# Kernel optimization log

Measured on AMD Instinct MI355X. Metric: run time of the kernel, lower is better.

## Reference

```python
import jax, jax.numpy as jnp
import numpy as np

N_NODES = 100_000
N_EDGES = 3_200_000
F_IN, F_HID, F_OUT = 128, 128, 128
MLP_HID, MLP_OUT = 256, 64


def setup_inputs() -> dict:
    key = jax.random.key(0)
    ks = jax.random.split(key, 11)
    def w(k, shape):
        fan_in = shape[0]
        return jax.random.normal(k, shape, jnp.float32) / jnp.sqrt(jnp.float32(fan_in))
    return {
        'x':   jax.random.normal(ks[0], (N_NODES, F_IN), jnp.float32),
        'src': jax.random.randint(ks[1], (N_EDGES,), 0, N_NODES, jnp.int32),
        'dst': jax.random.randint(ks[2], (N_EDGES,), 0, N_NODES, jnp.int32),
        'w1':  w(ks[3], (F_IN, F_HID)),  'b1': jnp.zeros((F_HID,), jnp.float32),
        'w2':  w(ks[4], (F_HID, F_OUT)), 'b2': jnp.zeros((F_OUT,), jnp.float32),
        'wm1': w(ks[5], (F_OUT, MLP_HID)), 'bm1': jnp.zeros((MLP_HID,), jnp.float32),
        'wm2': w(ks[6], (MLP_HID, MLP_OUT)), 'bm2': jnp.zeros((MLP_OUT,), jnp.float32),
    }


def reference(x, src, dst, w1, b1, w2, b2, wm1, bm1, wm2, bm2):
    n = x.shape[0]
    ones = jnp.ones(src.shape[0], x.dtype)
    # DGL GraphConv norm='both': clamp degrees to >=1, symmetric D^-1/2 A D^-1/2
    out_norm = jnp.clip(jax.ops.segment_sum(ones, src, num_segments=n), 1.0) ** -0.5
    in_norm = jnp.clip(jax.ops.segment_sum(ones, dst, num_segments=n), 1.0) ** -0.5

    def gconv(h, w, b):
        msg = (h * out_norm[:, None])[src]                       # [E, F] gather
        agg = jax.ops.segment_sum(msg, dst, num_segments=n)      # [N, F] scatter-add
        return (agg * in_norm[:, None]) @ w + b

    h = jax.nn.relu(gconv(x, w1, b1))   # conv1 + relu (dropout is identity in eval)
    h = jax.nn.relu(gconv(h, w2, b2))   # conv2 + relu
    h = jax.nn.relu(h @ wm1 + bm1)      # MLP hidden layer
    return h @ wm2 + bm2                # MLP output (no final activation)
```

## Files before the change

kernel.cpp:

```cpp
#include <hip/hip_runtime.h>
#include <hip/hip_bf16.h>
#include <cstdint>

__device__ __forceinline__ unsigned short f2b(float f) {
    union { float f; unsigned int i; } v; v.f = f;
    unsigned int i = v.i;
    unsigned int r = (i + 0x7FFFu + ((i >> 16) & 1u)) >> 16;
    return (unsigned short)r;
}
__device__ __forceinline__ float b2f_lo(unsigned int p) {
    union { unsigned int i; float f; } v; v.i = p << 16; return v.f;
}
__device__ __forceinline__ float b2f_hi(unsigned int p) {
    union { unsigned int i; float f; } v; v.i = p & 0xFFFF0000u; return v.f;
}
__device__ __forceinline__ unsigned int pack2(float a, float b) {
    return (unsigned int)f2b(a) | ((unsigned int)f2b(b) << 16);
}

typedef __attribute__((__ext_vector_type__(8))) __bf16 bf16x8;
typedef __attribute__((__ext_vector_type__(4))) float  f32x4;

#define N_NODES 100000
#define N_EDGES 3200000
#define NBUCK   400
#define BSZ     250

__global__ void k_hist2(const int* __restrict__ src, const int* __restrict__ dst,
                        int* __restrict__ gcntA, int* __restrict__ gcntB, int E) {
    __shared__ int hA[NBUCK], hB[NBUCK];
    int t = threadIdx.x;
    for (int j = t; j < NBUCK; j += 256) { hA[j] = 0; hB[j] = 0; }
    __syncthreads();
    for (int i = blockIdx.x * blockDim.x + t; i < E; i += gridDim.x * blockDim.x) {
        atomicAdd(&hA[dst[i] / BSZ], 1);
        atomicAdd(&hB[src[i] / BSZ], 1);
    }
    __syncthreads();
    for (int j = t; j < NBUCK; j += 256) {
        if (hA[j]) atomicAdd(&gcntA[j], hA[j]);
        if (hB[j]) atomicAdd(&gcntB[j], hB[j]);
    }
}

__global__ void k_scan_coarse(const int* __restrict__ gcntA, const int* __restrict__ gcntB,
                              int* __restrict__ gbaseA, int* __restrict__ gbaseB,
                              int* __restrict__ gcurA, int* __restrict__ gcurB,
                              int* __restrict__ offsets) {
    __shared__ int pA[512], pB[512];
    int t = threadIdx.x;
    int vA = (t < NBUCK) ? gcntA[t] : 0;
    int vB = (t < NBUCK) ? gcntB[t] : 0;
    pA[t] = vA; pB[t] = vB;
    __syncthreads();
    for (int d = 1; d < 512; d <<= 1) {
        int a = (t >= d) ? pA[t - d] : 0;
        int b = (t >= d) ? pB[t - d] : 0;
        __syncthreads();
        pA[t] += a; pB[t] += b;
        __syncthreads();
    }
    if (t < NBUCK) {
        gbaseA[t] = pA[t] - vA; gcurA[t] = pA[t] - vA;
        gbaseB[t] = pB[t] - vB; gcurB[t] = pB[t] - vB;
    }
    if (t == 511) {
        gbaseA[NBUCK] = pA[511];
        gbaseB[NBUCK] = pB[511];
        offsets[N_NODES] = pA[511];
    }
}

__global__ void k_scatter(const int* __restrict__ src, const int* __restrict__ dst,
                          int* __restrict__ gcurA, int* __restrict__ gcurB,
                          unsigned* __restrict__ pairs, unsigned short* __restrict__ keysB,
                          int E) {
    __shared__ int hA[NBUCK], hB[NBUCK], baA[NBUCK], baB[NBUCK], lcA[NBUCK], lcB[NBUCK];
    int t = threadIdx.x;
    const int CHUNK = 12500;
    int lo = blockIdx.x * CHUNK, hi = min(lo + CHUNK, E);
    for (int j = t; j < NBUCK; j += 256) { hA[j] = 0; hB[j] = 0; }
    __syncthreads();
    for (int i = lo + t; i < hi; i += 256) {
        atomicAdd(&hA[dst[i] / BSZ], 1);
        atomicAdd(&hB[src[i] / BSZ], 1);
    }
    __syncthreads();
    for (int j = t; j < NBUCK; j += 256) {
        baA[j] = hA[j] ? atomicAdd(&gcurA[j], hA[j]) : 0;
        lcA[j] = 0;
        baB[j] = hB[j] ? atomicAdd(&gcurB[j], hB[j]) : 0;
        lcB[j] = 0;
    }
    __syncthreads();
    for (int i = lo + t; i < hi; i += 256) {
        int s = src[i], d = dst[i];
        int bA = d / BSZ;
        int l  = atomicAdd(&lcA[bA], 1);
        pairs[baA[bA] + l] = ((unsigned)(d - bA * BSZ) << 17) | (unsigned)s;
        int bB = s / BSZ;
        int l2 = atomicAdd(&lcB[bB], 1);
        keysB[baB[bB] + l2] = (unsigned short)(s - bB * BSZ);
    }
}

__global__ void k_csr_bucket(const unsigned* __restrict__ pairs, const int* __restrict__ gbaseA,
                             int* __restrict__ offsets, float* __restrict__ in_norm,
                             int* __restrict__ esrc) {
    __shared__ int hist[256], scan[256], curs[256];
    int b = blockIdx.x, t = threadIdx.x;
    int node0 = b * BSZ;
    int bstart = gbaseA[b], bend = gbaseA[b + 1];
    if (t < 256) hist[t] = 0;
    __syncthreads();
    for (int i = bstart + t; i < bend; i += 512)
        atomicAdd(&hist[pairs[i] >> 17], 1);
    __syncthreads();
    if (t < 256) scan[t] = hist[t];
    __syncthreads();
    for (int d = 1; d < 256; d <<= 1) {
        int v = (t < 256 && t >= d) ? scan[t - d] : 0;
        __syncthreads();
        if (t < 256) scan[t] += v;
        __syncthreads();
    }
    if (t < BSZ) {
        int excl = scan[t] - hist[t];
        offsets[node0 + t] = bstart + excl;
        in_norm[node0 + t] = rsqrtf((float)max(hist[t], 1));
        curs[t] = excl;
    }
    __syncthreads();
    for (int i = bstart + t; i < bend; i += 512) {
        unsigned p = pairs[i];
        int d = (int)(p >> 17);
        int l = atomicAdd(&curs[d], 1);
        esrc[bstart + l] = (int)(p & 0x1FFFFu);
    }
}

__global__ void k_sortwave(const int* __restrict__ offsets, int* __restrict__ esrc, int N) {
    int node = blockIdx.x * 4 + (threadIdx.x >> 6);
    if (node >= N) return;
    int lane = threadIdx.x & 63;
    int lo = offsets[node], hi = offsets[node + 1];
    int len = hi - lo;
    if (len <= 1) return;
    const int INF = 0x7FFFFFFF;
    if (len <= 64) {
        int v0 = (lane < len) ? esrc[lo + lane] : INF;
#pragma unroll
        for (int k = 2; k <= 64; k <<= 1) {
#pragma unroll
            for (int d = 32; d > 0; d >>= 1) {
                if (d >= k) continue;
                int w0 = __shfl_xor(v0, d, 64);
                bool up = ((lane & k) == 0);
                bool lower = ((lane & d) == 0);
                v0 = (lower == up) ? min(v0, w0) : max(v0, w0);
            }
        }
        if (lane < len) esrc[lo + lane] = v0;
        return;
    }
    int v0 = (lane < len) ? esrc[lo + lane] : INF;
    int v1 = (64 + lane < len) ? esrc[lo + 64 + lane] : INF;
#pragma unroll
    for (int k = 2; k <= 128; k <<= 1) {
#pragma unroll
        for (int d = 64; d > 0; d >>= 1) {
            if (d >= k) continue;
            if (d == 64) {
                int a = min(v0, v1), b = max(v0, v1);
                v0 = a; v1 = b;
            } else {
                int w0 = __shfl_xor(v0, d, 64);
                int w1 = __shfl_xor(v1, d, 64);
                bool up0 = ((lane & k) == 0);
                bool up1 = (((64 + lane) & k) == 0);
                bool lower = ((lane & d) == 0);
                v0 = (lower == up0) ? min(v0, w0) : max(v0, w0);
                v1 = (lower == up1) ? min(v1, w1) : max(v1, w1);
            }
        }
    }
    if (lane < len) esrc[lo + lane] = v0;
    if (64 + lane < len) esrc[lo + 64 + lane] = v1;
}

__global__ void k_count_scale(const unsigned short* __restrict__ keys,
                              const int* __restrict__ gbaseB,
                              const float4* __restrict__ x4, float* __restrict__ out_norm,
                              uint2* __restrict__ xs) {
    __shared__ int hist[256];
    __shared__ float onl[BSZ];
    int b = blockIdx.x, t = threadIdx.x;
    int node0 = b * BSZ;
    int bstart = gbaseB[b], bend = gbaseB[b + 1];
    if (t < 256) hist[t] = 0;
    __syncthreads();
    for (int i = bstart + t; i < bend; i += 512)
        atomicAdd(&hist[keys[i]], 1);
    __syncthreads();
    if (t < BSZ) {
        float on = rsqrtf((float)max(hist[t], 1));
        onl[t] = on;
        out_norm[node0 + t] = on;
    }
    __syncthreads();
    size_t base4 = (size_t)node0 * 32;
    for (int i = t; i < BSZ * 32; i += 512) {
        float on = onl[i >> 5];
        float4 v = x4[base4 + i];
        uint2 o;
        o.x = pack2(v.x * on, v.y * on);
        o.y = pack2(v.z * on, v.w * on);
        xs[base4 + i] = o;
    }
}

__global__ void k_transpose4(const float* __restrict__ w1, const float* __restrict__ w2,
                             const float* __restrict__ wm1, const float* __restrict__ wm2,
                             unsigned short* __restrict__ t1, unsigned short* __restrict__ t2,
                             unsigned short* __restrict__ tm1, unsigned short* __restrict__ tm2) {
    int i = blockIdx.x * blockDim.x + threadIdx.x;
    const float* w; unsigned short* t; int N, idx;
    if (i < 16384)       { w = w1;  t = t1;  N = 128; idx = i; }
    else if (i < 32768)  { w = w2;  t = t2;  N = 128; idx = i - 16384; }
    else if (i < 65536)  { w = wm1; t = tm1; N = 256; idx = i - 32768; }
    else if (i < 81920)  { w = wm2; t = tm2; N = 64;  idx = i - 65536; }
    else return;
    int K = (i < 65536) ? 128 : 256;
    int k = idx / N, n = idx - k * N;
    t[(size_t)n * K + k] = f2b(w[idx]);
}

#define AGG_ADD(p)                                                              \
        a0 += b2f_lo(p.x); a1 += b2f_hi(p.x);                                   \
        a2 += b2f_lo(p.y); a3 += b2f_hi(p.y);                                   \
        a4 += b2f_lo(p.z); a5 += b2f_hi(p.z);                                   \
        a6 += b2f_lo(p.w); a7 += b2f_hi(p.w);

#define AGG_NODE_BODY(node)                                                     \
    int lo = offsets[node], hi = offsets[node + 1];                             \
    float a0 = 0.f, a1 = 0.f, a2 = 0.f, a3 = 0.f,                               \
          a4 = 0.f, a5 = 0.f, a6 = 0.f, a7 = 0.f;                               \
    int k = lo + g;                                                             \
    for (; k + 12 < hi; k += 16) {                                              \
        int s0 = esrc[k];                                                       \
        int s1 = esrc[k + 4];                                                   \
        int s2 = esrc[k + 8];                                                   \
        int s3 = esrc[k + 12];                                                  \
        uint4 p0 = feat[(size_t)s0 * 16 + c];                                   \
        uint4 p1 = feat[(size_t)s1 * 16 + c];                                   \
        uint4 p2 = feat[(size_t)s2 * 16 + c];                                   \
        uint4 p3 = feat[(size_t)s3 * 16 + c];                                   \
        AGG_ADD(p0) AGG_ADD(p1) AGG_ADD(p2) AGG_ADD(p3)                         \
    }                                                                           \
    for (; k < hi; k += 4) {                                                    \
        int s = esrc[k];                                                        \
        uint4 p = feat[(size_t)s * 16 + c];                                     \
        AGG_ADD(p)                                                              \
    }                                                                           \
    a0 += __shfl_xor(a0, 16, 64); a0 += __shfl_xor(a0, 32, 64);                 \
    a1 += __shfl_xor(a1, 16, 64); a1 += __shfl_xor(a1, 32, 64);                 \
    a2 += __shfl_xor(a2, 16, 64); a2 += __shfl_xor(a2, 32, 64);                 \
    a3 += __shfl_xor(a3, 16, 64); a3 += __shfl_xor(a3, 32, 64);                 \
    a4 += __shfl_xor(a4, 16, 64); a4 += __shfl_xor(a4, 32, 64);                 \
    a5 += __shfl_xor(a5, 16, 64); a5 += __shfl_xor(a5, 32, 64);                 \
    a6 += __shfl_xor(a6, 16, 64); a6 += __shfl_xor(a6, 32, 64);                 \
    a7 += __shfl_xor(a7, 16, 64); a7 += __shfl_xor(a7, 32, 64);

__global__ __launch_bounds__(256, 8)
void k_conv(const int* __restrict__ offsets, const int* __restrict__ esrc,
            const uint4* __restrict__ feat, const float* __restrict__ in_norm,
            const unsigned short* __restrict__ WT, const float* __restrict__ bias,
            const float* __restrict__ row_scale, unsigned short* __restrict__ C,
            int N) {
    __shared__ __align__(16) unsigned short A[32][136];
    int wv = threadIdx.x >> 6, lane = threadIdx.x & 63;
    int row0 = blockIdx.x * 32;
    int g = lane >> 4, c = lane & 15;

    for (int i = 0; i < 8; ++i) {
        int nl = wv * 8 + i;
        int node = row0 + nl;
        AGG_NODE_BODY(node)
        if (g == 0) {
            float inn = in_norm[node];
            uint4 o;
            o.x = pack2(a0 * inn, a1 * inn);
            o.y = pack2(a2 * inn, a3 * inn);
            o.z = pack2(a4 * inn, a5 * inn);
            o.w = pack2(a6 * inn, a7 * inn);
            *(uint4*)&A[nl][c * 8] = o;
        }
    }
    __syncthreads();

    int m = lane & 15, q = lane >> 4;
    const unsigned short* b0 = WT + (size_t)(wv * 32 + m) * 128 + q * 8;
    const unsigned short* b1 = b0 + (size_t)16 * 128;
    f32x4 acc00 = {0.f, 0.f, 0.f, 0.f}, acc10 = {0.f, 0.f, 0.f, 0.f};
    f32x4 acc01 = {0.f, 0.f, 0.f, 0.f}, acc11 = {0.f, 0.f, 0.f, 0.f};
#pragma unroll
    for (int k = 0; k < 128; k += 32) {
        bf16x8 bf0 = *(const bf16x8*)(b0 + k);
        bf16x8 bf1 = *(const bf16x8*)(b1 + k);
        bf16x8 af0 = *(const bf16x8*)&A[m][q * 8 + k];
        bf16x8 af1 = *(const bf16x8*)&A[16 + m][q * 8 + k];
        acc00 = __builtin_amdgcn_mfma_f32_16x16x32_bf16(af0, bf0, acc00, 0, 0, 0);
        acc10 = __builtin_amdgcn_mfma_f32_16x16x32_bf16(af1, bf0, acc10, 0, 0, 0);
        acc01 = __builtin_amdgcn_mfma_f32_16x16x32_bf16(af0, bf1, acc01, 0, 0, 0);
        acc11 = __builtin_amdgcn_mfma_f32_16x16x32_bf16(af1, bf1, acc11, 0, 0, 0);
    }
    __syncthreads();

    int col0 = wv * 32 + m;
    int col1 = col0 + 16;
    float bc0 = bias[col0], bc1 = bias[col1];
#pragma unroll
    for (int r = 0; r < 4; r++) {
        int rl = q * 4 + r;
        int rr = row0 + rl, rr1 = rr + 16;
        float v00 = fmaxf(acc00[r] + bc0, 0.f);
        float v10 = fmaxf(acc10[r] + bc0, 0.f);
        float v01 = fmaxf(acc01[r] + bc1, 0.f);
        float v11 = fmaxf(acc11[r] + bc1, 0.f);
        float s0 = row_scale[rr], s1 = row_scale[rr1];
        v00 *= s0; v01 *= s0; v10 *= s1; v11 *= s1;
        A[rl][col0]      = f2b(v00);
        A[rl][col1]      = f2b(v01);
        A[rl + 16][col0] = f2b(v10);
        A[rl + 16][col1] = f2b(v11);
    }
    __syncthreads();
#pragma unroll
    for (int it = 0; it < 2; ++it) {
        int idx = it * 256 + (int)threadIdx.x;
        int row = idx >> 4, seg = idx & 15;
        uint4 v = *(const uint4*)&A[row][seg * 8];
        *(uint4*)&C[(size_t)(row0 + row) * 128 + seg * 8] = v;
    }
}

__global__ __launch_bounds__(256, 8)
void k_conv2_mlp(const int* __restrict__ offsets, const int* __restrict__ esrc,
                 const uint4* __restrict__ feat, const float* __restrict__ in_norm,
                 const unsigned short* __restrict__ WT2, const float* __restrict__ b2,
                 const unsigned short* __restrict__ WTM1, const float* __restrict__ bm1,
                 const unsigned short* __restrict__ WTM2, const float* __restrict__ bm2,
                 float* __restrict__ out, int N) {
    __shared__ __align__(16) unsigned short smem[8704];
    unsigned short (*H1)[136] = (unsigned short(*)[136])(smem);
    unsigned short (*A)[136]  = (unsigned short(*)[136])(smem + 4352);
    unsigned short (*H2)[136] = (unsigned short(*)[136])(smem + 4352);

    int wv = threadIdx.x >> 6, lane = threadIdx.x & 63;
    int row0 = blockIdx.x * 32;
    int g = lane >> 4, c = lane & 15;

    for (int i = 0; i < 8; ++i) {
        int nl = wv * 8 + i;
        int node = row0 + nl;
        AGG_NODE_BODY(node)
        if (g == 0) {
            float inn = in_norm[node];
            uint4 o;
            o.x = pack2(a0 * inn, a1 * inn);
            o.y = pack2(a2 * inn, a3 * inn);
            o.z = pack2(a4 * inn, a5 * inn);
            o.w = pack2(a6 * inn, a7 * inn);
            *(uint4*)&A[nl][c * 8] = o;
        }
    }
    __syncthreads();

    int m = lane & 15, q = lane >> 4;

    {
        const unsigned short* bb0 = WT2 + (size_t)(wv * 32 + m) * 128 + q * 8;
        const unsigned short* bb1 = bb0 + (size_t)16 * 128;
        f32x4 acc00 = {0.f, 0.f, 0.f, 0.f}, acc10 = {0.f, 0.f, 0.f, 0.f};
        f32x4 acc01 = {0.f, 0.f, 0.f, 0.f}, acc11 = {0.f, 0.f, 0.f, 0.f};
#pragma unroll
        for (int k = 0; k < 128; k += 32) {
            bf16x8 bf0 = *(const bf16x8*)(bb0 + k);
            bf16x8 bf1 = *(const bf16x8*)(bb1 + k);
            bf16x8 af0 = *(const bf16x8*)&A[m][q * 8 + k];
            bf16x8 af1 = *(const bf16x8*)&A[16 + m][q * 8 + k];
            acc00 = __builtin_amdgcn_mfma_f32_16x16x32_bf16(af0, bf0, acc00, 0, 0, 0);
            acc10 = __builtin_amdgcn_mfma_f32_16x16x32_bf16(af1, bf0, acc10, 0, 0, 0);
            acc01 = __builtin_amdgcn_mfma_f32_16x16x32_bf16(af0, bf1, acc01, 0, 0, 0);
            acc11 = __builtin_amdgcn_mfma_f32_16x16x32_bf16(af1, bf1, acc11, 0, 0, 0);
        }
        int col0 = wv * 32 + m;
        int col1 = col0 + 16;
        float bc0 = b2[col0], bc1 = b2[col1];
#pragma unroll
        for (int r = 0; r < 4; r++) {
            int rl = q * 4 + r;
            H1[rl][col0]      = f2b(fmaxf(acc00[r] + bc0, 0.f));
            H1[rl][col1]      = f2b(fmaxf(acc01[r] + bc1, 0.f));
            H1[rl + 16][col0] = f2b(fmaxf(acc10[r] + bc0, 0.f));
            H1[rl + 16][col1] = f2b(fmaxf(acc11[r] + bc1, 0.f));
        }
    }
    __syncthreads();

    f32x4 macc0 = {0.f, 0.f, 0.f, 0.f}, macc1 = {0.f, 0.f, 0.f, 0.f};
    int colo = wv * 16 + m;
    const unsigned short* bp2 = WTM2 + (size_t)colo * 256 + q * 8;
#pragma unroll
    for (int half = 0; half < 2; ++half) {
#pragma unroll
        for (int cb = 0; cb < 2; cb++) {
            int colh = half * 128 + wv * 32 + cb * 16 + m;
            const unsigned short* bp = WTM1 + (size_t)colh * 128 + q * 8;
            f32x4 acc0 = {0.f, 0.f, 0.f, 0.f};
            f32x4 acc1 = {0.f, 0.f, 0.f, 0.f};
#pragma unroll
            for (int s = 0; s < 4; s++) {
                bf16x8 bfr = *(const bf16x8*)(bp + s * 32);
                bf16x8 ha0 = *(const bf16x8*)&H1[m][s * 32 + q * 8];
                bf16x8 ha1 = *(const bf16x8*)&H1[m + 16][s * 32 + q * 8];
                acc0 = __builtin_amdgcn_mfma_f32_16x16x32_bf16(ha0, bfr, acc0, 0, 0, 0);
                acc1 = __builtin_amdgcn_mfma_f32_16x16x32_bf16(ha1, bfr, acc1, 0, 0, 0);
            }
            float bc = bm1[colh];
            int cl = colh & 127;
#pragma unroll
            for (int r = 0; r < 4; r++) {
                H2[q * 4 + r][cl]      = f2b(fmaxf(acc0[r] + bc, 0.f));
                H2[q * 4 + r + 16][cl] = f2b(fmaxf(acc1[r] + bc, 0.f));
            }
        }
        __syncthreads();
#pragma unroll
        for (int s = 0; s < 4; s++) {
            bf16x8 bfr = *(const bf16x8*)(bp2 + half * 128 + s * 32);
            bf16x8 ha0 = *(const bf16x8*)&H2[m][s * 32 + q * 8];
            bf16x8 ha1 = *(const bf16x8*)&H2[m + 16][s * 32 + q * 8];
            macc0 = __builtin_amdgcn_mfma_f32_16x16x32_bf16(ha0, bfr, macc0, 0, 0, 0);
            macc1 = __builtin_amdgcn_mfma_f32_16x16x32_bf16(ha1, bfr, macc1, 0, 0, 0);
        }
        __syncthreads();
    }

    float* OS = (float*)smem;
    float bc = bm2[colo];
#pragma unroll
    for (int r = 0; r < 4; r++) {
        OS[(q * 4 + r) * 64 + colo]        = macc0[r] + bc;
        OS[(q * 4 + r + 16) * 64 + colo]   = macc1[r] + bc;
    }
    __syncthreads();
#pragma unroll
    for (int it = 0; it < 2; ++it) {
        int idx = it * 256 + (int)threadIdx.x;
        int row = idx >> 4, seg = idx & 15;
        float4 v = *(const float4*)&OS[row * 64 + seg * 4];
        *(float4*)&out[(size_t)(row0 + row) * 64 + seg * 4] = v;
    }
}

extern "C" void kernel_launch(void* const* d_in, const int* in_sizes, int n_in,
                              void* d_out, int out_size, void* d_ws, size_t ws_size,
                              hipStream_t stream) {
    const float* x    = (const float*)d_in[0];
    const int*   src  = (const int*)d_in[1];
    const int*   dst  = (const int*)d_in[2];
    const float* w1   = (const float*)d_in[3];
    const float* b1   = (const float*)d_in[4];
    const float* w2   = (const float*)d_in[5];
    const float* b2   = (const float*)d_in[6];
    const float* wm1  = (const float*)d_in[7];
    const float* bm1  = (const float*)d_in[8];
    const float* wm2  = (const float*)d_in[9];
    const float* bm2  = (const float*)d_in[10];

    const int N = N_NODES;
    const int E = N_EDGES;

    char* p = (char*)d_ws;
    auto alloc = [&](size_t bytes) -> void* {
        void* r = (void*)p;
        p += (bytes + 255) & ~(size_t)255;
        return r;
    };
    int*   gcntA   = (int*)alloc((NBUCK + 1) * 4);
    int*   gcntB   = (int*)alloc((NBUCK + 1) * 4);
    int*   gbaseA  = (int*)alloc((NBUCK + 1) * 4);
    int*   gbaseB  = (int*)alloc((NBUCK + 1) * 4);
    int*   gcurA   = (int*)alloc((NBUCK + 1) * 4);
    int*   gcurB   = (int*)alloc((NBUCK + 1) * 4);
    int*   offsets = (int*)alloc((size_t)(N + 1) * 4);
    float* out_norm = (float*)alloc((size_t)N * 4);
    float* in_norm  = (float*)alloc((size_t)N * 4);
    int*   esrc     = (int*)alloc((size_t)E * 4);
    unsigned int* bufA = (unsigned int*)alloc((size_t)N * 128 * 2);
    unsigned int* bufB = (unsigned int*)alloc((size_t)N * 128 * 2);
    unsigned int* bufC = (unsigned int*)alloc((size_t)N * 128 * 2);
    unsigned short* wt1  = (unsigned short*)alloc(128 * 128 * 2);
    unsigned short* wt2  = (unsigned short*)alloc(128 * 128 * 2);
    unsigned short* wtm1 = (unsigned short*)alloc(256 * 128 * 2);
    unsigned short* wtm2 = (unsigned short*)alloc(64 * 256 * 2);
    (void)ws_size; (void)n_in; (void)in_sizes; (void)out_size;

    unsigned*       pairs = (unsigned*)bufB;
    unsigned short* keysB = (unsigned short*)bufC;

    hipMemsetAsync(gcntA, 0, (size_t)((char*)gcntB - (char*)gcntA) + NBUCK * 4, stream);

    const int TB = 256;
    k_hist2<<<dim3(256), dim3(TB), 0, stream>>>(src, dst, gcntA, gcntB, E);
    k_scan_coarse<<<dim3(1), dim3(512), 0, stream>>>(gcntA, gcntB, gbaseA, gbaseB,
                                                     gcurA, gcurB, offsets);
    k_scatter<<<dim3(256), dim3(TB), 0, stream>>>(src, dst, gcurA, gcurB, pairs, keysB, E);
    k_csr_bucket<<<dim3(NBUCK), dim3(512), 0, stream>>>(pairs, gbaseA, offsets, in_norm, esrc);
    k_sortwave<<<dim3(N / 4), dim3(TB), 0, stream>>>(offsets, esrc, N);
    k_count_scale<<<dim3(NBUCK), dim3(512), 0, stream>>>(
        keysB, gbaseB, (const float4*)x, out_norm, (uint2*)bufA);

    k_transpose4<<<dim3(320), dim3(TB), 0, stream>>>(w1, w2, wm1, wm2, wt1, wt2, wtm1, wtm2);

    k_conv<<<dim3(N / 32), dim3(TB), 0, stream>>>(
        offsets, esrc, (const uint4*)bufA, in_norm, wt1, b1, out_norm,
        (unsigned short*)bufC, N);

    k_conv2_mlp<<<dim3(N / 32), dim3(TB), 0, stream>>>(
        offsets, esrc, (const uint4*)bufC, in_norm, wt2, b2, wtm1, bm1, wtm2, bm2,
        (float*)d_out, N);
}
```

Measured before the change: 552.6 us.

## Fuse per-node sort into CSR bucket kernel and reuse per-chunk histograms

k_hist2 now processes fixed chunks and saves per-block bucket histograms, so k_scatter no longer recomputes them from src/dst. The CSR bucket kernel stages each bucket's edges in LDS, bitonic-sorts each node's list there and writes esrc once, which removes the separate global sort pass. The weight transpose is folded into k_count_scale and the final output uses nontemporal stores. Risks: the LDS bucket capacity (BCAP 9216) is not checked against the actual bucket size, the large LDS buffer may lower occupancy, and nodes with degree over 128 are still only partly sorted.

```diff
diff --git a/kernel.cpp b/kernel.cpp
--- a/kernel.cpp
+++ b/kernel.cpp
@@ -25,19 +25,26 @@
 #define N_EDGES 3200000
 #define NBUCK   400
 #define BSZ     250
+#define NCHUNK  256
+#define CHUNK   12500
+#define BCAP    9216
 
 __global__ void k_hist2(const int* __restrict__ src, const int* __restrict__ dst,
-                        int* __restrict__ gcntA, int* __restrict__ gcntB, int E) {
+                        int* __restrict__ gcntA, int* __restrict__ gcntB,
+                        int* __restrict__ blkA, int* __restrict__ blkB, int E) {
     __shared__ int hA[NBUCK], hB[NBUCK];
-    int t = threadIdx.x;
+    int t = threadIdx.x, b = blockIdx.x;
+    int lo = b * CHUNK, hi = min(lo + CHUNK, E);
     for (int j = t; j < NBUCK; j += 256) { hA[j] = 0; hB[j] = 0; }
     __syncthreads();
-    for (int i = blockIdx.x * blockDim.x + t; i < E; i += gridDim.x * blockDim.x) {
+    for (int i = lo + t; i < hi; i += 256) {
         atomicAdd(&hA[dst[i] / BSZ], 1);
         atomicAdd(&hB[src[i] / BSZ], 1);
     }
     __syncthreads();
     for (int j = t; j < NBUCK; j += 256) {
+        blkA[b * NBUCK + j] = hA[j];
+        blkB[b * NBUCK + j] = hB[j];
         if (hA[j]) atomicAdd(&gcntA[j], hA[j]);
         if (hB[j]) atomicAdd(&gcntB[j], hB[j]);
     }
@@ -73,23 +80,18 @@
 
 __global__ void k_scatter(const int* __restrict__ src, const int* __restrict__ dst,
                           int* __restrict__ gcurA, int* __restrict__ gcurB,
+                          const int* __restrict__ blkA, const int* __restrict__ blkB,
                           unsigned* __restrict__ pairs, unsigned short* __restrict__ keysB,
                           int E) {
-    __shared__ int hA[NBUCK], hB[NBUCK], baA[NBUCK], baB[NBUCK], lcA[NBUCK], lcB[NBUCK];
-    int t = threadIdx.x;
-    const int CHUNK = 12500;
-    int lo = blockIdx.x * CHUNK, hi = min(lo + CHUNK, E);
-    for (int j = t; j < NBUCK; j += 256) { hA[j] = 0; hB[j] = 0; }
-    __syncthreads();
-    for (int i = lo + t; i < hi; i += 256) {
-        atomicAdd(&hA[dst[i] / BSZ], 1);
-        atomicAdd(&hB[src[i] / BSZ], 1);
-    }
-    __syncthreads();
+    __shared__ int baA[NBUCK], baB[NBUCK], lcA[NBUCK], lcB[NBUCK];
+    int t = threadIdx.x, b = blockIdx.x;
+    int lo = b * CHUNK, hi = min(lo + CHUNK, E);
     for (int j = t; j < NBUCK; j += 256) {
-        baA[j] = hA[j] ? atomicAdd(&gcurA[j], hA[j]) : 0;
+        int hA = blkA[b * NBUCK + j];
+        baA[j] = hA ? atomicAdd(&gcurA[j], hA) : 0;
         lcA[j] = 0;
-        baB[j] = hB[j] ? atomicAdd(&gcurB[j], hB[j]) : 0;
+        int hB = blkB[b * NBUCK + j];
+        baB[j] = hB ? atomicAdd(&gcurB[j], hB) : 0;
         lcB[j] = 0;
     }
     __syncthreads();
@@ -104,13 +106,16 @@
     }
 }
 
-__global__ void k_csr_bucket(const unsigned* __restrict__ pairs, const int* __restrict__ gbaseA,
-                             int* __restrict__ offsets, float* __restrict__ in_norm,
-                             int* __restrict__ esrc) {
+__global__ __launch_bounds__(512)
+void k_csr_sort(const unsigned* __restrict__ pairs, const int* __restrict__ gbaseA,
+                int* __restrict__ offsets, float* __restrict__ in_norm,
+                int* __restrict__ esrc) {
+    __shared__ int el[BCAP];
     __shared__ int hist[256], scan[256], curs[256];
     int b = blockIdx.x, t = threadIdx.x;
     int node0 = b * BSZ;
     int bstart = gbaseA[b], bend = gbaseA[b + 1];
+    int cnt = bend - bstart;
     if (t < 256) hist[t] = 0;
     __syncthreads();
     for (int i = bstart + t; i < bend; i += 512)
@@ -135,63 +140,81 @@
         unsigned p = pairs[i];
         int d = (int)(p >> 17);
         int l = atomicAdd(&curs[d], 1);
-        esrc[bstart + l] = (int)(p & 0x1FFFFu);
-    }
-}
-
-__global__ void k_sortwave(const int* __restrict__ offsets, int* __restrict__ esrc, int N) {
-    int node = blockIdx.x * 4 + (threadIdx.x >> 6);
-    if (node >= N) return;
-    int lane = threadIdx.x & 63;
-    int lo = offsets[node], hi = offsets[node + 1];
-    int len = hi - lo;
-    if (len <= 1) return;
+        el[l] = (int)(p & 0x1FFFFu);
+    }
+    __syncthreads();
+    int wv = t >> 6, lane = t & 63;
     const int INF = 0x7FFFFFFF;
-    if (len <= 64) {
-        int v0 = (lane < len) ? esrc[lo + lane] : INF;
-#pragma unroll
-        for (int k = 2; k <= 64; k <<= 1) {
-#pragma unroll
-            for (int d = 32; d > 0; d >>= 1) {
-                if (d >= k) continue;
-                int w0 = __shfl_xor(v0, d, 64);
-                bool up = ((lane & k) == 0);
-                bool lower = ((lane & d) == 0);
-                v0 = (lower == up) ? min(v0, w0) : max(v0, w0);
+    for (int n = wv; n < BSZ; n += 8) {
+        int len = hist[n];
+        if (len <= 1) continue;
+        int base = scan[n] - len;
+        if (len <= 64) {
+            int v0 = (lane < len) ? el[base + lane] : INF;
+#pragma unroll
+            for (int k = 2; k <= 64; k <<= 1) {
+#pragma unroll
+                for (int d = 32; d > 0; d >>= 1) {
+                    if (d >= k) continue;
+                    int w0 = __shfl_xor(v0, d, 64);
+                    bool up = ((lane & k) == 0);
+                    bool lower = ((lane & d) == 0);
+                    v0 = (lower == up) ? min(v0, w0) : max(v0, w0);
+                }
             }
-        }
-        if (lane < len) esrc[lo + lane] = v0;
-        return;
-    }
-    int v0 = (lane < len) ? esrc[lo + lane] : INF;
-    int v1 = (64 + lane < len) ? esrc[lo + 64 + lane] : INF;
-#pragma unroll
-    for (int k = 2; k <= 128; k <<= 1) {
-#pragma unroll
-        for (int d = 64; d > 0; d >>= 1) {
-            if (d >= k) continue;
-            if (d == 64) {
-                int a = min(v0, v1), b = max(v0, v1);
-                v0 = a; v1 = b;
-            } else {
-                int w0 = __shfl_xor(v0, d, 64);
-                int w1 = __shfl_xor(v1, d, 64);
-                bool up0 = ((lane & k) == 0);
-                bool up1 = (((64 + lane) & k) == 0);
-                bool lower = ((lane & d) == 0);
-                v0 = (lower == up0) ? min(v0, w0) : max(v0, w0);
-                v1 = (lower == up1) ? min(v1, w1) : max(v1, w1);
+            if (lane < len) el[base + lane] = v0;
+        } else {
+            int v0 = (lane < len) ? el[base + lane] : INF;
+            int v1 = (64 + lane < len) ? el[base + 64 + lane] : INF;
+#pragma unroll
+            for (int k = 2; k <= 128; k <<= 1) {
+#pragma unroll
+                for (int d = 64; d > 0; d >>= 1) {
+                    if (d >= k) continue;
+                    if (d == 64) {
+                        int a = min(v0, v1), bb = max(v0, v1);
+                        v0 = a; v1 = bb;
+                    } else {
+                        int w0 = __shfl_xor(v0, d, 64);
+                        int w1 = __shfl_xor(v1, d, 64);
+                        bool up0 = ((lane & k) == 0);
+                        bool up1 = (((64 + lane) & k) == 0);
+                        bool lower = ((lane & d) == 0);
+                        v0 = (lower == up0) ? min(v0, w0) : max(v0, w0);
+                        v1 = (lower == up1) ? min(v1, w1) : max(v1, w1);
+                    }
+                }
             }
-        }
-    }
-    if (lane < len) esrc[lo + lane] = v0;
-    if (64 + lane < len) esrc[lo + 64 + lane] = v1;
-}
-
-__global__ void k_count_scale(const unsigned short* __restrict__ keys,
-                              const int* __restrict__ gbaseB,
-                              const float4* __restrict__ x4, float* __restrict__ out_norm,
-                              uint2* __restrict__ xs) {
+            if (lane < len) el[base + lane] = v0;
+            if (64 + lane < len) el[base + 64 + lane] = v1;
+        }
+    }
+    __syncthreads();
+    for (int i = t; i < cnt; i += 512) esrc[bstart + i] = el[i];
+}
+
+__global__ __launch_bounds__(512)
+void k_count_scale(const unsigned short* __restrict__ keys,
+                   const int* __restrict__ gbaseB,
+                   const float4* __restrict__ x4, float* __restrict__ out_norm,
+                   uint2* __restrict__ xs,
+                   const float* __restrict__ w1, const float* __restrict__ w2,
+                   const float* __restrict__ wm1, const float* __restrict__ wm2,
+                   unsigned short* __restrict__ t1, unsigned short* __restrict__ t2,
+                   unsigned short* __restrict__ tm1, unsigned short* __restrict__ tm2) {
+    {
+        int gid = blockIdx.x * 512 + threadIdx.x;
+        if (gid < 81920) {
+            const float* w; unsigned short* tt; int Nn, idx;
+            if (gid < 16384)       { w = w1;  tt = t1;  Nn = 128; idx = gid; }
+            else if (gid < 32768)  { w = w2;  tt = t2;  Nn = 128; idx = gid - 16384; }
+            else if (gid < 65536)  { w = wm1; tt = tm1; Nn = 256; idx = gid - 32768; }
+            else                   { w = wm2; tt = tm2; Nn = 64;  idx = gid - 65536; }
+            int K = (gid < 65536) ? 128 : 256;
+            int k = idx / Nn, n = idx - k * Nn;
+            tt[(size_t)n * K + k] = f2b(w[idx]);
+        }
+    }
     __shared__ int hist[256];
     __shared__ float onl[BSZ];
     int b = blockIdx.x, t = threadIdx.x;
@@ -217,22 +240,6 @@
         o.y = pack2(v.z * on, v.w * on);
         xs[base4 + i] = o;
     }
-}
-
-__global__ void k_transpose4(const float* __restrict__ w1, const float* __restrict__ w2,
-                             const float* __restrict__ wm1, const float* __restrict__ wm2,
-                             unsigned short* __restrict__ t1, unsigned short* __restrict__ t2,
-                             unsigned short* __restrict__ tm1, unsigned short* __restrict__ tm2) {
-    int i = blockIdx.x * blockDim.x + threadIdx.x;
-    const float* w; unsigned short* t; int N, idx;
-    if (i < 16384)       { w = w1;  t = t1;  N = 128; idx = i; }
-    else if (i < 32768)  { w = w2;  t = t2;  N = 128; idx = i - 16384; }
-    else if (i < 65536)  { w = wm1; t = tm1; N = 256; idx = i - 32768; }
-    else if (i < 81920)  { w = wm2; t = tm2; N = 64;  idx = i - 65536; }
-    else return;
-    int K = (i < 65536) ? 128 : 256;
-    int k = idx / N, n = idx - k * N;
-    t[(size_t)n * K + k] = f2b(w[idx]);
 }
 
 #define AGG_ADD(p)                                                              \
@@ -459,8 +466,8 @@
     for (int it = 0; it < 2; ++it) {
         int idx = it * 256 + (int)threadIdx.x;
         int row = idx >> 4, seg = idx & 15;
-        float4 v = *(const float4*)&OS[row * 64 + seg * 4];
-        *(float4*)&out[(size_t)(row0 + row) * 64 + seg * 4] = v;
+        f32x4 v = *(const f32x4*)&OS[row * 64 + seg * 4];
+        __builtin_nontemporal_store(v, (f32x4*)&out[(size_t)(row0 + row) * 64 + seg * 4]);
     }
 }
 
@@ -494,6 +501,8 @@
     int*   gbaseB  = (int*)alloc((NBUCK + 1) * 4);
     int*   gcurA   = (int*)alloc((NBUCK + 1) * 4);
     int*   gcurB   = (int*)alloc((NBUCK + 1) * 4);
+    int*   blkA    = (int*)alloc((size_t)NCHUNK * NBUCK * 4);
+    int*   blkB    = (int*)alloc((size_t)NCHUNK * NBUCK * 4);
     int*   offsets = (int*)alloc((size_t)(N + 1) * 4);
     float* out_norm = (float*)alloc((size_t)N * 4);
     float* in_norm  = (float*)alloc((size_t)N * 4);
@@ -510,19 +519,18 @@
     unsigned*       pairs = (unsigned*)bufB;
     unsigned short* keysB = (unsigned short*)bufC;
 
-    hipMemsetAsync(gcntA, 0, (size_t)((char*)gcntB - (char*)gcntA) + NBUCK * 4, stream);
+    (void)hipMemsetAsync(gcntA, 0, (size_t)((char*)gcntB - (char*)gcntA) + NBUCK * 4, stream);
 
     const int TB = 256;
-    k_hist2<<<dim3(256), dim3(TB), 0, stream>>>(src, dst, gcntA, gcntB, E);
+    k_hist2<<<dim3(NCHUNK), dim3(TB), 0, stream>>>(src, dst, gcntA, gcntB, blkA, blkB, E);
     k_scan_coarse<<<dim3(1), dim3(512), 0, stream>>>(gcntA, gcntB, gbaseA, gbaseB,
                                                      gcurA, gcurB, offsets);
-    k_scatter<<<dim3(256), dim3(TB), 0, stream>>>(src, dst, gcurA, gcurB, pairs, keysB, E);
-    k_csr_bucket<<<dim3(NBUCK), dim3(512), 0, stream>>>(pairs, gbaseA, offsets, in_norm, esrc);
-    k_sortwave<<<dim3(N / 4), dim3(TB), 0, stream>>>(offsets, esrc, N);
+    k_scatter<<<dim3(NCHUNK), dim3(TB), 0, stream>>>(src, dst, gcurA, gcurB, blkA, blkB,
+                                                     pairs, keysB, E);
+    k_csr_sort<<<dim3(NBUCK), dim3(512), 0, stream>>>(pairs, gbaseA, offsets, in_norm, esrc);
     k_count_scale<<<dim3(NBUCK), dim3(512), 0, stream>>>(
-        keysB, gbaseB, (const float4*)x, out_norm, (uint2*)bufA);
-
-    k_transpose4<<<dim3(320), dim3(TB), 0, stream>>>(w1, w2, wm1, wm2, wt1, wt2, wtm1, wtm2);
+        keysB, gbaseB, (const float4*)x, out_norm, (uint2*)bufA,
+        w1, w2, wm1, wm2, wt1, wt2, wtm1, wtm2);
 
     k_conv<<<dim3(N / 32), dim3(TB), 0, stream>>>(
         offsets, esrc, (const uint4*)bufA, in_norm, wt1, b1, out_norm,
```

New measurement: 525.9 us. -4.8%, faster.
